# Kernel tuning notes

Hardware: AMD Instinct MI355X
Metric: run time of the kernel (lower is better)

## Reference

```python
import jax, jax.numpy as jnp
import numpy as np
from jax import lax

B, CIN, H, W = 64, 3, 224, 224
FEAT = 64          # conv output channels after pooling
OUT = 1024         # output_dim


def _conv2d(x, w, b, stride):
    # x: NCHW, w: OIHW, padding=1, stride=stride
    y = lax.conv_general_dilated(
        x, w, window_strides=(stride, stride), padding=((1, 1), (1, 1)),
        dimension_numbers=("NCHW", "OIHW", "NCHW"))
    return y + b[None, :, None, None]


def setup_inputs() -> dict:
    key = jax.random.key(0)
    ks = jax.random.split(key, 12)
    s = 0.05
    return {
        "x": jax.random.normal(ks[0], (B, CIN, H, W), dtype=jnp.float32),
        "w1": jax.random.normal(ks[1], (32, CIN, 3, 3), dtype=jnp.float32) * s,
        "b1": jax.random.normal(ks[2], (32,), dtype=jnp.float32) * s,
        "w2": jax.random.normal(ks[3], (64, 32, 3, 3), dtype=jnp.float32) * s,
        "b2": jax.random.normal(ks[4], (64,), dtype=jnp.float32) * s,
        "wm": jax.random.normal(ks[5], (OUT, FEAT), dtype=jnp.float32) * s,
        "bm": jax.random.normal(ks[6], (OUT,), dtype=jnp.float32) * s,
        "wc": jax.random.normal(ks[7], (OUT, FEAT * FEAT), dtype=jnp.float32) * s,
        "bc": jax.random.normal(ks[8], (OUT,), dtype=jnp.float32) * s,
        "w3": jax.random.normal(ks[9], (OUT, FEAT ** 3), dtype=jnp.float32) * s,
        "b3": jax.random.normal(ks[10], (OUT,), dtype=jnp.float32) * s,
    }


def reference(x, w1, b1, w2, b2, wm, bm, wc, bc, w3, b3):
    # conv trunk: conv3x3 s2 -> relu -> conv3x3 s2 -> relu -> global avg pool
    h = jax.nn.relu(_conv2d(x, w1, b1, 2))
    h = jax.nn.relu(_conv2d(h, w2, b2, 2))
    feat = jnp.mean(h, axis=(2, 3))                    # (B, 64)

    mean_feat = feat @ wm.T + bm                       # (B, OUT)

    fc = feat - jnp.mean(feat, axis=1, keepdims=True)  # centered (B, 64)

    # 2nd-order: outer product flattened -> linear
    cov = (fc[:, :, None] * fc[:, None, :]).reshape(B, FEAT * FEAT)
    cov_feat = cov @ wc.T + bc

    # 3rd-order: rank-1 third-order outer product flattened -> linear
    outer3 = (fc[:, :, None, None] * fc[:, None, :, None] * fc[:, None, None, :])
    third_feat = outer3.reshape(B, FEAT ** 3) @ w3.T + b3

    return mean_feat + cov_feat + third_feat
```

## Files before the change

kernel.cpp:

```cpp
#include <hip/hip_runtime.h>
#include <hip/hip_bf16.h>

#define BB   64
#define CIN  3
#define HH   224
#define WW   224
#define C1   32
#define H1   112
#define W1   112
#define C2   64
#define H2   56
#define W2   56
#define FEATN 64
#define OUTN 1024
#define K3TOT (FEATN*FEATN*FEATN)

typedef __bf16 bf16x8 __attribute__((ext_vector_type(8)));
typedef float  f32x4  __attribute__((ext_vector_type(4)));
typedef unsigned int u32;

__device__ __forceinline__ void gload_lds16(const void* g, void* l) {
  __builtin_amdgcn_global_load_lds((const __attribute__((address_space(1))) u32*)g,
                                   (__attribute__((address_space(3))) u32*)l, 16, 0, 0);
}
__device__ __forceinline__ void gload_lds16_nt(const void* g, void* l) {
  __builtin_amdgcn_global_load_lds((const __attribute__((address_space(1))) u32*)g,
                                   (__attribute__((address_space(3))) u32*)l, 16, 0, 2);
}

__global__ __launch_bounds__(256) void conv1_kernel(const float* __restrict__ x,
        const float* __restrict__ w1, const float* __restrict__ b1,
        __bf16* __restrict__ h1T, const float* __restrict__ w2,
        __bf16* __restrict__ wf) {
    int gid = blockIdx.x * 256 + threadIdx.x;

    if (gid < 64 * 452) {
      int b = gid / 452, s = gid - b * 452;
      int row, col;
      if      (s < 114) { row = 0;        col = s; }
      else if (s < 228) { row = 113;      col = s - 114; }
      else if (s < 340) { row = s - 227;  col = 0; }
      else              { row = s - 339;  col = 113; }
      __bf16* p = h1T + (((size_t)b * 114 + row) * 114 + col) * 32;
      bf16x8 z = {};
      #pragma unroll
      for (int k = 0; k < 4; ++k) *(bf16x8*)(p + k * 8) = z;
    } else if (gid < 64 * 452 + 18432) {
      int t = gid - 64 * 452;
      int e    = t & 7;
      int lane = (t >> 3) & 63;
      int q    = (t >> 9) % 9;
      int j    = t / 4608;
      int oc = j * 16 + (lane & 15);
      int c  = (lane >> 4) * 8 + e;
      wf[t] = (__bf16)w2[(oc * C1 + c) * 9 + q];
    }

    int pos = gid;
    int b   = pos / (H1 * 56);
    int rem = pos - b * (H1 * 56);
    int oy  = rem / 56;
    int g   = rem - oy * 56;
    int iy0 = oy * 2 - 1;

    float win[CIN][3][5];
    #pragma unroll
    for (int c = 0; c < CIN; ++c)
      #pragma unroll
      for (int dy = 0; dy < 3; ++dy) {
        int iy = iy0 + dy;
        bool rv = (iy >= 0) & (iy < HH);
        const float* row = x + ((size_t)(b * CIN + c) * HH + (rv ? iy : 0)) * WW;
        float lf = (rv && g > 0) ? row[4 * g - 1] : 0.f;
        float4 f4 = rv ? *(const float4*)(row + 4 * g) : (float4){0.f, 0.f, 0.f, 0.f};
        win[c][dy][0] = lf;
        win[c][dy][1] = f4.x; win[c][dy][2] = f4.y;
        win[c][dy][3] = f4.z; win[c][dy][4] = f4.w;
      }

    float acc[2][C1];
    #pragma unroll
    for (int u = 0; u < 2; ++u)
      #pragma unroll
      for (int oc = 0; oc < C1; ++oc) acc[u][oc] = b1[oc];

    #pragma unroll
    for (int c = 0; c < CIN; ++c)
      #pragma unroll
      for (int dy = 0; dy < 3; ++dy)
        #pragma unroll
        for (int dx = 0; dx < 3; ++dx) {
          float w0 = win[c][dy][dx];
          float w1v = win[c][dy][dx + 2];
          const float* wq = w1 + c * 9 + dy * 3 + dx;
          #pragma unroll
          for (int oc = 0; oc < C1; ++oc) {
            float wv = wq[oc * 27];
            acc[0][oc] = fmaf(wv, w0, acc[0][oc]);
            acc[1][oc] = fmaf(wv, w1v, acc[1][oc]);
          }
        }

    __bf16* dst = h1T + (((size_t)b * 114 + oy + 1) * 114 + (2 * g) + 1) * 32;
    #pragma unroll
    for (int u = 0; u < 2; ++u) {
      bf16x8 outv[4];
      #pragma unroll
      for (int k = 0; k < 32; ++k)
        outv[k >> 3][k & 7] = (__bf16)fmaxf(acc[u][k], 0.f);
      #pragma unroll
      for (int k = 0; k < 4; ++k) *(bf16x8*)(dst + u * 32 + k * 8) = outv[k];
    }
}

__global__ __launch_bounds__(256) void conv2_kernel(const __bf16* __restrict__ h1T,
        const __bf16* __restrict__ wf, const float* __restrict__ b2,
        float* __restrict__ featp) {
    __shared__ __align__(16) char tile[2304 * 16];
    __shared__ float pool_red[4][64];
    int t = threadIdx.x;
    int bid = blockIdx.x;
    int b  = bid / 28;
    int yt = bid - b * 28;
    int y0 = yt * 2;
    int w = t >> 6, lane = t & 63, l15 = lane & 15, l4 = lane >> 4;

    const char* src_base = (const char*)(h1T + ((size_t)b * 114 + 2 * y0) * 114 * 32);
    #pragma unroll
    for (int i = 0; i < 9; ++i) {
      int g = (w * 9 + i) * 64 + lane;
      int site = g >> 2; site = site < 569 ? site : 569;
      int qp = g & 3;
      int r5 = site / 114;
      int col = site - r5 * 114;
      int ql = (qp - col) & 3;
      gload_lds16(src_base + (size_t)site * 64 + ql * 16, tile + (size_t)g * 16);
    }
    __syncthreads();

    int sbase[2], urot[2];
    #pragma unroll
    for (int p = 0; p < 2; ++p) {
      int mt = 2 * w + p;
      int yl = mt >> 2;
      int xl = ((mt & 3) << 4) + l15;
      int xe = xl < 55 ? xl : 55;
      sbase[p] = ((yl * 2) * 114 + 2 * xe) * 64;
      urot[p]  = (l4 + 2 * xe) & 3;
    }

    f32x4 acc[2][4];
    #pragma unroll
    for (int p = 0; p < 2; ++p)
      #pragma unroll
      for (int j = 0; j < 4; ++j) acc[p][j] = (f32x4){0.f, 0.f, 0.f, 0.f};

    #pragma unroll
    for (int q = 0; q < 9; ++q) {
      int dy = q / 3, dx = q % 3;
      bf16x8 bw[4];
      #pragma unroll
      for (int j = 0; j < 4; ++j)
        bw[j] = *(const bf16x8*)(wf + ((j * 9 + q) * 64 + lane) * 8);
      bf16x8 af[2];
      #pragma unroll
      for (int p = 0; p < 2; ++p) {
        int addr = sbase[p] + (dy * 114 + dx) * 64 + (((urot[p] + dx) & 3) << 4);
        af[p] = *(const bf16x8*)(tile + addr);
      }
      #pragma unroll
      for (int p = 0; p < 2; ++p)
        #pragma unroll
        for (int j = 0; j < 4; ++j)
          acc[p][j] = __builtin_amdgcn_mfma_f32_16x16x32_bf16(af[p], bw[j], acc[p][j], 0, 0, 0);
    }

    float bias[4];
    #pragma unroll
    for (int j = 0; j < 4; ++j) bias[j] = b2[j * 16 + l15];
    float ps[4] = {0.f, 0.f, 0.f, 0.f};
    #pragma unroll
    for (int p = 0; p < 2; ++p) {
      int mt = 2 * w + p;
      bool valid = ((mt & 3) != 3) || (l4 < 2);
      #pragma unroll
      for (int j = 0; j < 4; ++j) {
        float sj = 0.f;
        #pragma unroll
        for (int r = 0; r < 4; ++r)
          sj += fmaxf(acc[p][j][r] + bias[j], 0.f);
        ps[j] += valid ? sj : 0.f;
      }
    }
    #pragma unroll
    for (int j = 0; j < 4; ++j) {
      ps[j] += __shfl_xor(ps[j], 16);
      ps[j] += __shfl_xor(ps[j], 32);
    }
    if (l4 == 0) {
      #pragma unroll
      for (int j = 0; j < 4; ++j) pool_red[w][j * 16 + l15] = ps[j];
    }
    __syncthreads();
    if (t < 64) {
      float s = pool_red[0][t] + pool_red[1][t] + pool_red[2][t] + pool_red[3][t];
      featp[((size_t)yt * 64 + b) * 64 + t] = s;
    }
}

__global__ __launch_bounds__(64) void center2_kernel(const float* __restrict__ featp,
        float* __restrict__ featN, float* __restrict__ fc) {
    int b = blockIdx.x;
    int c = threadIdx.x;
    float s = 0.f;
    #pragma unroll 7
    for (int yt = 0; yt < 28; ++yt)
      s += featp[((size_t)yt * 64 + b) * 64 + c];
    s *= (1.f / (H2 * W2));
    float tot = s;
    #pragma unroll
    for (int off = 32; off; off >>= 1) tot += __shfl_xor(tot, off);
    featN[b * 64 + c] = s;
    fc[b * 64 + c]    = s - tot * (1.f / 64.f);
}

#define T3_NCH 128

struct T3S {
    float stage[2][2][16][64];
    float fcT[64][66];
    float wred[2][64];
};

__global__ __launch_bounds__(128) void third_kernel(const float* __restrict__ fc,
        const float* __restrict__ w3, float* __restrict__ thrd) {
    __shared__ __align__(16) T3S sh;
    int t = threadIdx.x;
    int w = t >> 6, lane = t & 63, l15 = lane & 15, l4 = lane >> 4;
    int o = blockIdx.x;
    int swz = (l15 & 7) << 4;

    for (int idx = t; idx < 4096; idx += 128)
      sh.fcT[idx & 63][idx >> 6] = fc[idx];

    const char* seg = (const char*)w3 + ((size_t)o << 20) + (size_t)w * 524288;

    #pragma unroll
    for (int ii = 0; ii < 4; ++ii) {
      int row = ii * 4 + (lane >> 4);
      int lo  = (lane & 15) * 16;
      gload_lds16_nt(seg + row * 256 + (lo ^ ((row & 7) << 4)),
                     (char*)&sh.stage[w][0][0][0] + ii * 1024);
    }

    bf16x8 bfrag[2][4];
    #pragma unroll
    for (int ks = 0; ks < 2; ++ks)
      #pragma unroll
      for (int nt = 0; nt < 4; ++nt) {
        const float* p = fc + (nt * 16 + l15) * 64 + ks * 32 + l4 * 8;
        float4 v0 = *(const float4*)p;
        float4 v1 = *(const float4*)(p + 4);
        bfrag[ks][nt][0] = (__bf16)v0.x; bfrag[ks][nt][1] = (__bf16)v0.y;
        bfrag[ks][nt][2] = (__bf16)v0.z; bfrag[ks][nt][3] = (__bf16)v0.w;
        bfrag[ks][nt][4] = (__bf16)v1.x; bfrag[ks][nt][5] = (__bf16)v1.y;
        bfrag[ks][nt][6] = (__bf16)v1.z; bfrag[ks][nt][7] = (__bf16)v1.w;
      }

    __syncthreads();

    float oacc[4] = {0.f, 0.f, 0.f, 0.f};

    #pragma unroll 1
    for (int c = 0; c < T3_NCH; ++c) {
      if (c + 1 < T3_NCH) {
        const char* s2 = seg + (size_t)(c + 1) * 4096;
        char* db = (char*)&sh.stage[w][(c + 1) & 1][0][0];
        #pragma unroll
        for (int ii = 0; ii < 4; ++ii) {
          int row = ii * 4 + (lane >> 4);
          int lo  = (lane & 15) * 16;
          gload_lds16_nt(s2 + row * 256 + (lo ^ ((row & 7) << 4)), db + ii * 1024);
        }
        asm volatile("s_waitcnt vmcnt(4)" ::: "memory");
      } else {
        asm volatile("s_waitcnt vmcnt(0)" ::: "memory");
      }
      __builtin_amdgcn_sched_barrier(0);

      const char* cb = (const char*)&sh.stage[w][c & 1][0][0];
      f32x4 acc[4];
      #pragma unroll
      for (int nt = 0; nt < 4; ++nt) acc[nt] = (f32x4){0.f, 0.f, 0.f, 0.f};
      #pragma unroll
      for (int ks = 0; ks < 2; ++ks) {
        int off0 = l15 * 256 + ((ks * 128 + l4 * 32) ^ swz);
        float4 a0 = *(const float4*)(cb + off0);
        float4 a1 = *(const float4*)(cb + (off0 ^ 16));
        bf16x8 af;
        af[0] = (__bf16)a0.x; af[1] = (__bf16)a0.y;
        af[2] = (__bf16)a0.z; af[3] = (__bf16)a0.w;
        af[4] = (__bf16)a1.x; af[5] = (__bf16)a1.y;
        af[6] = (__bf16)a1.z; af[7] = (__bf16)a1.w;
        #pragma unroll
        for (int nt = 0; nt < 4; ++nt)
          acc[nt] = __builtin_amdgcn_mfma_f32_16x16x32_bf16(af, bfrag[ks][nt], acc[nt], 0, 0, 0);
      }
      int i = w * 32 + (c >> 2);
      #pragma unroll
      for (int nt = 0; nt < 4; ++nt) {
        int b = nt * 16 + l15;
        float s = 0.f;
        #pragma unroll
        for (int r = 0; r < 4; ++r) {
          int j = (c * 16 + l4 * 4 + r) & 63;
          s = fmaf(sh.fcT[j][b], acc[nt][r], s);
        }
        oacc[nt] = fmaf(sh.fcT[i][b], s, oacc[nt]);
      }
    }

    #pragma unroll
    for (int nt = 0; nt < 4; ++nt) {
      oacc[nt] += __shfl_xor(oacc[nt], 16);
      oacc[nt] += __shfl_xor(oacc[nt], 32);
    }
    if (l4 == 0) {
      #pragma unroll
      for (int nt = 0; nt < 4; ++nt) sh.wred[w][nt * 16 + l15] = oacc[nt];
    }
    __syncthreads();
    if (t < 64) thrd[o * 64 + t] = sh.wred[0][t] + sh.wred[1][t];
}

__global__ __launch_bounds__(256) void finale_kernel(const float* __restrict__ feat,
        const float* __restrict__ fc,
        const float* __restrict__ wm, const float* __restrict__ bm,
        const float* __restrict__ wc, const float* __restrict__ bcv,
        const float* __restrict__ b3, const float* __restrict__ thrd,
        float* __restrict__ out) {
    __shared__ float featT[FEATN * FEATN];
    __shared__ float fcT[FEATN * FEATN];
    int t = threadIdx.x;
    for (int i = t; i < FEATN * FEATN; i += 256) {
      int b = i >> 6, c = i & 63;
      featT[c*64 + b] = feat[i];
      fcT[c*64 + b]   = fc[i];
    }
    __syncthreads();

    int b = t & 63;
    int o = blockIdx.x * 4 + (t >> 6);

    float fr[64];
    #pragma unroll
    for (int c4 = 0; c4 < 16; ++c4) {
      float4 v = *(const float4*)(fc + b*64 + c4*4);
      fr[c4*4+0]=v.x; fr[c4*4+1]=v.y; fr[c4*4+2]=v.z; fr[c4*4+3]=v.w;
    }

    float acc = bm[o] + bcv[o] + b3[o];
    #pragma unroll 8
    for (int c = 0; c < FEATN; ++c)
      acc = fmaf(featT[c*64 + b], wm[o*FEATN + c], acc);

    const float* wcrow = wc + (size_t)o * (FEATN * FEATN);
    #pragma unroll 1
    for (int c1 = 0; c1 < 64; ++c1) {
      float a2 = 0.f;
      #pragma unroll
      for (int c2 = 0; c2 < 64; ++c2)
        a2 = fmaf(fr[c2], wcrow[c1*64 + c2], a2);
      acc = fmaf(fcT[c1*64 + b], a2, acc);
    }

    out[b * OUTN + o] = acc + thrd[o * 64 + b];
}

extern "C" void kernel_launch(void* const* d_in, const int* in_sizes, int n_in,
                              void* d_out, int out_size, void* d_ws, size_t ws_size,
                              hipStream_t stream) {
    const float* x   = (const float*)d_in[0];
    const float* w1  = (const float*)d_in[1];
    const float* b1  = (const float*)d_in[2];
    const float* w2  = (const float*)d_in[3];
    const float* b2  = (const float*)d_in[4];
    const float* wm  = (const float*)d_in[5];
    const float* bm  = (const float*)d_in[6];
    const float* wc  = (const float*)d_in[7];
    const float* bcv = (const float*)d_in[8];
    const float* w3  = (const float*)d_in[9];
    const float* b3  = (const float*)d_in[10];
    float* out = (float*)d_out;

    float* ws    = (float*)d_ws;
    __bf16* h1T  = (__bf16*)ws;
    float* featp = ws + 13307904;
    float* featN = ws + 13422592;
    float* fcv   = ws + 13426688;
    float* thrd  = ws + 13430784;
    __bf16* wfrg = (__bf16*)(ws + 13496320);

    conv1_kernel  <<<1568, 256, 0, stream>>>(x, w1, b1, h1T, w2, wfrg);
    conv2_kernel  <<<1792, 256, 0, stream>>>(h1T, wfrg, b2, featp);
    center2_kernel<<<64,   64,  0, stream>>>(featp, featN, fcv);
    third_kernel  <<<1024, 128, 0, stream>>>(fcv, w3, thrd);
    finale_kernel <<<256,  256, 0, stream>>>(featN, fcv, wm, bm, wc, bcv, b3, thrd, out);
}
```

Measured before the change: 291.0 us.

## Fuse centering into conv2 via last-block atomic, finale into third kernel

The separate center kernel is removed. The last conv2 block, detected through an atomic counter, now reduces the pooled partials and writes the centered features and per-batch means. The finale kernel is also folded into the third-order kernel's epilogue: each block computes the mean and covariance terms for its output column using the centered features already in shared memory, with the mean term rebuilt from fc plus the per-batch mean times the row sum of wm. This removes two kernel launches and the thrd round trip through memory. In exchange, a single block does the serial centering reduction, and the wc reads now sit on the tail of the third kernel.

```diff
diff --git a/kernel.cpp b/kernel.cpp
--- a/kernel.cpp
+++ b/kernel.cpp
@@ -31,8 +31,9 @@
 __global__ __launch_bounds__(256) void conv1_kernel(const float* __restrict__ x,
         const float* __restrict__ w1, const float* __restrict__ b1,
         __bf16* __restrict__ h1T, const float* __restrict__ w2,
-        __bf16* __restrict__ wf) {
+        __bf16* __restrict__ wf, unsigned* __restrict__ cnt) {
     int gid = blockIdx.x * 256 + threadIdx.x;
+    if (gid == 0) *cnt = 0u;
 
     if (gid < 64 * 452) {
       int b = gid / 452, s = gid - b * 452;
@@ -113,11 +114,14 @@
     }
 }
 
+#define CONV2_GRID 1792
 __global__ __launch_bounds__(256) void conv2_kernel(const __bf16* __restrict__ h1T,
         const __bf16* __restrict__ wf, const float* __restrict__ b2,
-        float* __restrict__ featp) {
+        float* __restrict__ featp, float* __restrict__ fcv,
+        float* __restrict__ fmean, unsigned* __restrict__ cnt) {
     __shared__ __align__(16) char tile[2304 * 16];
     __shared__ float pool_red[4][64];
+    __shared__ unsigned lastf;
     int t = threadIdx.x;
     int bid = blockIdx.x;
     int b  = bid / 28;
@@ -206,22 +210,39 @@
       float s = pool_red[0][t] + pool_red[1][t] + pool_red[2][t] + pool_red[3][t];
       featp[((size_t)yt * 64 + b) * 64 + t] = s;
     }
-}
-
-__global__ __launch_bounds__(64) void center2_kernel(const float* __restrict__ featp,
-        float* __restrict__ featN, float* __restrict__ fc) {
-    int b = blockIdx.x;
-    int c = threadIdx.x;
-    float s = 0.f;
-    #pragma unroll 7
-    for (int yt = 0; yt < 28; ++yt)
-      s += featp[((size_t)yt * 64 + b) * 64 + c];
-    s *= (1.f / (H2 * W2));
-    float tot = s;
-    #pragma unroll
-    for (int off = 32; off; off >>= 1) tot += __shfl_xor(tot, off);
-    featN[b * 64 + c] = s;
-    fc[b * 64 + c]    = s - tot * (1.f / 64.f);
+
+    __threadfence();
+    if (t == 0) {
+      unsigned v = __hip_atomic_fetch_add(cnt, 1u, __ATOMIC_ACQ_REL,
+                                          __HIP_MEMORY_SCOPE_AGENT);
+      lastf = (v == CONV2_GRID - 1) ? 1u : 0u;
+    }
+    __syncthreads();
+    if (lastf) {
+      int bb = t >> 2, cq = (t & 3) * 16;
+      float s[16];
+      #pragma unroll
+      for (int i = 0; i < 16; ++i) s[i] = 0.f;
+      #pragma unroll 4
+      for (int ytt = 0; ytt < 28; ++ytt) {
+        const float* p = featp + ((size_t)ytt * 64 + bb) * 64 + cq;
+        #pragma unroll
+        for (int q4 = 0; q4 < 4; ++q4) {
+          float4 v4 = *(const float4*)(p + q4 * 4);
+          s[q4*4+0] += v4.x; s[q4*4+1] += v4.y;
+          s[q4*4+2] += v4.z; s[q4*4+3] += v4.w;
+        }
+      }
+      float tot = 0.f;
+      #pragma unroll
+      for (int i = 0; i < 16; ++i) { s[i] *= (1.f / (H2 * W2)); tot += s[i]; }
+      tot += __shfl_xor(tot, 1);
+      tot += __shfl_xor(tot, 2);
+      float mean = tot * (1.f / 64.f);
+      #pragma unroll
+      for (int i = 0; i < 16; ++i) fcv[bb * 64 + cq + i] = s[i] - mean;
+      if ((t & 3) == 0) fmean[bb] = mean;
+    }
 }
 
 #define T3_NCH 128
@@ -230,10 +251,15 @@
     float stage[2][2][16][64];
     float fcT[64][66];
     float wred[2][64];
+    float epi[2][64];
 };
 
 __global__ __launch_bounds__(128) void third_kernel(const float* __restrict__ fc,
-        const float* __restrict__ w3, float* __restrict__ thrd) {
+        const float* __restrict__ w3,
+        const float* __restrict__ wm, const float* __restrict__ bm,
+        const float* __restrict__ wc, const float* __restrict__ bcv,
+        const float* __restrict__ b3, const float* __restrict__ fmean,
+        float* __restrict__ out) {
     __shared__ __align__(16) T3S sh;
     int t = threadIdx.x;
     int w = t >> 6, lane = t & 63, l15 = lane & 15, l4 = lane >> 4;
@@ -247,8 +273,8 @@
 
     #pragma unroll
     for (int ii = 0; ii < 4; ++ii) {
-      int row = ii * 4 + (lane >> 4);
-      int lo  = (lane & 15) * 16;
+      int row = ii * 4 + l4;
+      int lo  = l15 * 16;
       gload_lds16_nt(seg + row * 256 + (lo ^ ((row & 7) << 4)),
                      (char*)&sh.stage[w][0][0][0] + ii * 1024);
     }
@@ -278,8 +304,8 @@
         char* db = (char*)&sh.stage[w][(c + 1) & 1][0][0];
         #pragma unroll
         for (int ii = 0; ii < 4; ++ii) {
-          int row = ii * 4 + (lane >> 4);
-          int lo  = (lane & 15) * 16;
+          int row = ii * 4 + l4;
+          int lo  = l15 * 16;
           gload_lds16_nt(s2 + row * 256 + (lo ^ ((row & 7) << 4)), db + ii * 1024);
         }
         asm volatile("s_waitcnt vmcnt(4)" ::: "memory");
@@ -330,51 +356,39 @@
       for (int nt = 0; nt < 4; ++nt) sh.wred[w][nt * 16 + l15] = oacc[nt];
     }
     __syncthreads();
-    if (t < 64) thrd[o * 64 + t] = sh.wred[0][t] + sh.wred[1][t];
-}
-
-__global__ __launch_bounds__(256) void finale_kernel(const float* __restrict__ feat,
-        const float* __restrict__ fc,
-        const float* __restrict__ wm, const float* __restrict__ bm,
-        const float* __restrict__ wc, const float* __restrict__ bcv,
-        const float* __restrict__ b3, const float* __restrict__ thrd,
-        float* __restrict__ out) {
-    __shared__ float featT[FEATN * FEATN];
-    __shared__ float fcT[FEATN * FEATN];
-    int t = threadIdx.x;
-    for (int i = t; i < FEATN * FEATN; i += 256) {
-      int b = i >> 6, c = i & 63;
-      featT[c*64 + b] = feat[i];
-      fcT[c*64 + b]   = fc[i];
-    }
-    __syncthreads();
-
-    int b = t & 63;
-    int o = blockIdx.x * 4 + (t >> 6);
-
-    float fr[64];
-    #pragma unroll
-    for (int c4 = 0; c4 < 16; ++c4) {
-      float4 v = *(const float4*)(fc + b*64 + c4*4);
-      fr[c4*4+0]=v.x; fr[c4*4+1]=v.y; fr[c4*4+2]=v.z; fr[c4*4+3]=v.w;
-    }
-
-    float acc = bm[o] + bcv[o] + b3[o];
+
+    int eb = t & 63;
+    const float* wcrow = wc + (size_t)o * 4096;
+    const float* wmrow = wm + o * 64;
+    float fm = fmean[eb];
+    float covp = 0.f, meanp = 0.f, wmsump = 0.f;
+    #pragma unroll 1
+    for (int c1 = w * 32; c1 < w * 32 + 32; ++c1) {
+      float a2 = 0.f;
+      #pragma unroll
+      for (int c2 = 0; c2 < 64; c2 += 4) {
+        float4 wv = *(const float4*)(wcrow + c1 * 64 + c2);
+        a2 = fmaf(sh.fcT[c2 + 0][eb], wv.x, a2);
+        a2 = fmaf(sh.fcT[c2 + 1][eb], wv.y, a2);
+        a2 = fmaf(sh.fcT[c2 + 2][eb], wv.z, a2);
+        a2 = fmaf(sh.fcT[c2 + 3][eb], wv.w, a2);
+      }
+      covp = fmaf(sh.fcT[c1][eb], a2, covp);
+    }
     #pragma unroll 8
-    for (int c = 0; c < FEATN; ++c)
-      acc = fmaf(featT[c*64 + b], wm[o*FEATN + c], acc);
-
-    const float* wcrow = wc + (size_t)o * (FEATN * FEATN);
-    #pragma unroll 1
-    for (int c1 = 0; c1 < 64; ++c1) {
-      float a2 = 0.f;
-      #pragma unroll
-      for (int c2 = 0; c2 < 64; ++c2)
-        a2 = fmaf(fr[c2], wcrow[c1*64 + c2], a2);
-      acc = fmaf(fcT[c1*64 + b], a2, acc);
-    }
-
-    out[b * OUTN + o] = acc + thrd[o * 64 + b];
+    for (int c = w * 32; c < w * 32 + 32; ++c) {
+      float wmv = wmrow[c];
+      meanp = fmaf(sh.fcT[c][eb], wmv, meanp);
+      wmsump += wmv;
+    }
+    sh.epi[w][eb] = covp + meanp + fm * wmsump;
+    __syncthreads();
+    if (t < 64) {
+      float res = bm[o] + bcv[o] + b3[o]
+                + sh.epi[0][t] + sh.epi[1][t]
+                + sh.wred[0][t] + sh.wred[1][t];
+      out[t * OUTN + o] = res;
+    }
 }
 
 extern "C" void kernel_launch(void* const* d_in, const int* in_sizes, int n_in,
@@ -396,14 +410,12 @@
     float* ws    = (float*)d_ws;
     __bf16* h1T  = (__bf16*)ws;
     float* featp = ws + 13307904;
-    float* featN = ws + 13422592;
-    float* fcv   = ws + 13426688;
-    float* thrd  = ws + 13430784;
-    __bf16* wfrg = (__bf16*)(ws + 13496320);
-
-    conv1_kernel  <<<1568, 256, 0, stream>>>(x, w1, b1, h1T, w2, wfrg);
-    conv2_kernel  <<<1792, 256, 0, stream>>>(h1T, wfrg, b2, featp);
-    center2_kernel<<<64,   64,  0, stream>>>(featp, featN, fcv);
-    third_kernel  <<<1024, 128, 0, stream>>>(fcv, w3, thrd);
-    finale_kernel <<<256,  256, 0, stream>>>(featN, fcv, wm, bm, wc, bcv, b3, thrd, out);
-}
+    float* fcv   = ws + 13422592;
+    float* fmean = ws + 13426688;
+    __bf16* wfrg = (__bf16*)(ws + 13430784);
+    unsigned* cnt = (unsigned*)(ws + 13440000);
+
+    conv1_kernel<<<1568, 256, 0, stream>>>(x, w1, b1, h1T, w2, wfrg, cnt);
+    conv2_kernel<<<CONV2_GRID, 256, 0, stream>>>(h1T, wfrg, b2, featp, fcv, fmean, cnt);
+    third_kernel<<<1024, 128, 0, stream>>>(fcv, w3, wm, bm, wc, bcv, b3, fmean, out);
+}
```

Result: slower. 403.5 us (+38.7%).
